# Kernel optimization log

Hardware: AMD Instinct MI355X
Metric: run time of the kernel (lower is better)

The kernel has to match this reference:

```python
import jax, jax.numpy as jnp
import numpy as np

N = 4096          # total ensemble boxes per frame
M = 20            # MAX_MERGE_NUMS
H = 16            # MergeNet hidden_c
COND_THRES = 0.2
IOU_THRES = 0.3


def setup_inputs() -> dict:
    key = jax.random.key(0)
    ks = jax.random.split(key, 6)
    u = jax.random.uniform(ks[0], (N, 9), dtype=jnp.float32)
    # realistic lidar boxes: centers in a ~140x80x8m range, dims in [0.5, 4.5), heading in [-pi, pi)
    centers = (u[:, 0:3] - 0.5) * jnp.array([140.0, 80.0, 8.0], jnp.float32)
    dims = u[:, 3:6] * 4.0 + 0.5
    heading = (u[:, 6:7] - 0.5) * (2.0 * np.pi)
    extra = u[:, 7:9]  # extra box attrs (cols 7:9), untouched by merge
    pred_boxes = jnp.concatenate([centers, dims, heading, extra], axis=-1)
    pred_scores = jax.random.uniform(ks[1], (N,), dtype=jnp.float32)
    pred_labels = jax.random.randint(ks[2], (N,), 0, 3)
    w1 = (jax.random.normal(ks[3], (M, H), jnp.float32) / np.sqrt(M)).astype(jnp.float32)
    b1 = jnp.zeros((H,), jnp.float32)
    w2 = (jax.random.normal(ks[4], (H, H), jnp.float32) / np.sqrt(H)).astype(jnp.float32)
    b2 = jnp.zeros((H,), jnp.float32)
    w3 = (jax.random.normal(ks[5], (H, 1), jnp.float32) / np.sqrt(H)).astype(jnp.float32)
    b3 = jnp.zeros((1,), jnp.float32)
    return dict(pred_boxes=pred_boxes, pred_scores=pred_scores, pred_labels=pred_labels,
                w1=w1, b1=b1, w2=w2, b2=b2, w3=w3, b3=b3)


def _bev_aligned(b):
    # boxes3d_lidar_to_aligned_bev_boxes: swap dx/dy when |limit_period(heading)| >= pi/4
    ang = b[..., 6] - jnp.floor(b[..., 6] / np.pi + 0.5) * np.pi
    swap = jnp.abs(ang) >= (np.pi / 4)
    dx = jnp.where(swap, b[..., 4], b[..., 3])
    dy = jnp.where(swap, b[..., 3], b[..., 4])
    return jnp.stack([b[..., 0] - dx / 2, b[..., 1] - dy / 2,
                      b[..., 0] + dx / 2, b[..., 1] + dy / 2], axis=-1)


def _iou_one_many(a, b):
    # axis-aligned BEV IoU of one box a[4] vs many b[N,4]
    xmin = jnp.maximum(a[0], b[:, 0]); ymin = jnp.maximum(a[1], b[:, 1])
    xmax = jnp.minimum(a[2], b[:, 2]); ymax = jnp.minimum(a[3], b[:, 3])
    inter = jnp.maximum(xmax - xmin, 0.0) * jnp.maximum(ymax - ymin, 0.0)
    area_a = (a[2] - a[0]) * (a[3] - a[1])
    area_b = (b[:, 2] - b[:, 0]) * (b[:, 3] - b[:, 1])
    return inter / jnp.maximum(area_a + area_b - inter, 1e-6)


def _nms_merge(pred_boxes, pred_scores, pred_labels, w1, b1, w2, b2, w3, b3):
    valid = pred_scores > COND_THRES
    sort_key = jnp.where(valid, pred_scores, -jnp.inf)
    order = jnp.argsort(-sort_key)                 # descending by score; invalid sink
    boxes9 = pred_boxes[order]
    labels = pred_labels[order]
    scores = pred_scores[order]
    suppressed0 = ~valid[order]
    boxes7 = boxes9[:, :7]
    bev0 = _bev_aligned(boxes7)                    # merged boxes get suppressed, so bev is static

    def mergenet(ob):                              # ob: [M, 7] -> merged box [7]
        x = ob.T                                   # [7, M] (k is the feature axis)
        h = jax.nn.relu(x @ w1 + b1)
        h = jax.nn.relu(h @ w2 + b2)
        return (h @ w3 + b3)[:, 0]

    def step(suppressed, i):
        active = ~suppressed[i]
        same = (labels == labels[i]) & (~suppressed)
        iou = _iou_one_many(bev0[i], bev0)         # [N]
        over = (iou > IOU_THRES) & same            # includes self (iou=1)
        count = jnp.sum(over)
        rank = jnp.cumsum(over) - 1                # slot of each overlap, in score order
        tgt = jnp.where(over & (rank < M), rank, M)
        ob = jnp.zeros((M, 7), boxes7.dtype).at[tgt].set(boxes7, mode='drop')
        bi = boxes7[i]
        new_box = jnp.where(count > 1, mergenet(ob), bi)
        new_box = new_box.at[3:6].set(jnp.maximum(new_box[3:6], 1e-5))
        out_box = jnp.where(active, new_box, bi)
        return suppressed | (over & active), (out_box, active)

    _, (merged7, keep) = jax.lax.scan(step, suppressed0, jnp.arange(N))
    out_boxes = jnp.concatenate([merged7, boxes9[:, 7:9]], axis=-1)   # [N, 9]
    return out_boxes, scores, labels, keep


def reference(pred_boxes, pred_scores, pred_labels, w1, b1, w2, b2, w3, b3):
    # Returns fixed-shape (boxes9, scores, labels, keep_mask); rows with keep=False
    # correspond to boxes that torch's dynamic version would have removed.
    return _nms_merge(pred_boxes, pred_scores, pred_labels, w1, b1, w2, b2, w3, b3)
```

## Files before the change

### kernel.cpp

```cpp
#include <hip/hip_runtime.h>
#include <cstdint>

typedef unsigned long long u64;
typedef unsigned int u32;

#define NB 4096
#define NW 64
#define MM 20
#define HH 16
#define COND_THRES 0.2f
#define IOU_THRES 0.3f
#define PI_F  3.14159265358979323846f
#define PI4_F 0.78539816339744830962f

#define WS_KEPT    0
#define WS_MASK    32768
#define WS_BOX9S   (WS_MASK + NB*NW*8)
#define WS_BEVS    (WS_BOX9S + NB*9*4)
#define WS_SCORES  (WS_BEVS + NB*16)
#define WS_LABELS  (WS_SCORES + NB*4)
#define WS_NBRW    (WS_LABELS + NB*4)
#define WS_SUPSTEP (WS_NBRW + NB*8)

__device__ __forceinline__ u64 sort_key(float s, int i) {
  u32 sb = (s > COND_THRES) ? __float_as_uint(s) : 0u;
  return ((u64)(sb ^ 0xFFFFFFFFu) << 12) | (u64)i;
}

__global__ void __launch_bounds__(256) k_prep(const float* __restrict__ scores,
                                              const float* __restrict__ boxes9,
                                              const int* __restrict__ labels,
                                              float* __restrict__ box9s, float4* __restrict__ bevs,
                                              float* __restrict__ scoress, int* __restrict__ labelss,
                                              u64* __restrict__ nbrw) {
  #pragma clang fp contract(off)
  __shared__ u64 keys[NB];
  __shared__ u32 part[16][16];
  int tid = threadIdx.x;
  for (int k = tid; k < NB; k += 256) keys[k] = sort_key(scores[k], k);
  __syncthreads();
  int bl = tid & 15;
  int ch = tid >> 4;
  u64 ki = keys[blockIdx.x * 16 + bl];
  int c = 0;
  #pragma unroll 16
  for (int t = 0; t < 256; ++t) c += (keys[(ch << 8) + t] < ki) ? 1 : 0;
  part[bl][ch] = (u32)c;
  __syncthreads();
  if (tid < 16) {
    int i = blockIdx.x * 16 + tid;
    int r = 0;
    #pragma unroll
    for (int q = 0; q < 16; ++q) r += (int)part[tid][q];
    nbrw[i] = 0;
    float b[9];
    #pragma unroll
    for (int f = 0; f < 9; ++f) b[f] = boxes9[i * 9 + f];
    #pragma unroll
    for (int f = 0; f < 9; ++f) box9s[r * 9 + f] = b[f];
    float ang = b[6] - floorf(b[6] / PI_F + 0.5f) * PI_F;
    bool sw = fabsf(ang) >= PI4_F;
    float dx = sw ? b[4] : b[3];
    float dy = sw ? b[3] : b[4];
    bevs[r] = make_float4(b[0] - dx * 0.5f, b[1] - dy * 0.5f,
                          b[0] + dx * 0.5f, b[1] + dy * 0.5f);
    scoress[r] = scores[i];
    labelss[r] = labels[i];
  }
}

__global__ void __launch_bounds__(64) k_mask(const float4* __restrict__ bevs,
                                             const int* __restrict__ labelss,
                                             const float* __restrict__ scoress,
                                             u64* __restrict__ mask,
                                             u64* __restrict__ nbrw) {
  #pragma clang fp contract(off)
  __shared__ float4 bj[64];
  __shared__ int lj[64];
  __shared__ u64 tw[64];
  int t = threadIdx.x;
  int b = blockIdx.x;
  int it = (int)((sqrtf(8.0f * (float)b + 1.0f) - 1.0f) * 0.5f);
  while ((it + 1) * (it + 2) / 2 <= b) ++it;
  while (it * (it + 1) / 2 > b) --it;
  int jt = b - it * (it + 1) / 2;
  int j = jt * 64 + t;
  bj[t] = bevs[j];
  lj[t] = labelss[j];
  u64 vj = __ballot(scoress[j] > COND_THRES);
  int i = it * 64 + t;
  float4 a = bevs[i];
  int la = labelss[i];
  float area_a = (a.z - a.x) * (a.w - a.y);
  __syncthreads();
  u64 w = 0;
  #pragma unroll 8
  for (int kk = 0; kk < 64; ++kk) {
    float4 bb = bj[kk];
    float xmin = fmaxf(a.x, bb.x), ymin = fmaxf(a.y, bb.y);
    float xmax = fminf(a.z, bb.z), ymax = fminf(a.w, bb.w);
    float inter = fmaxf(xmax - xmin, 0.0f) * fmaxf(ymax - ymin, 0.0f);
    float area_b = (bb.z - bb.x) * (bb.w - bb.y);
    float iou = inter / fmaxf(area_a + area_b - inter, 1e-6f);
    if ((iou > IOU_THRES) && (la == lj[kk])) w |= (1ull << kk);
  }
  mask[(u64)i * NW + jt] = w;
  {
    u64 below = (jt < it) ? ~0ull : ((1ull << t) - 1ull);
    if (w & vj & below) atomicOr(&nbrw[i], 1ull << jt);
  }
  if (jt < it) {
    tw[t] = w;
    __syncthreads();
    u64 wT = 0;
    #pragma unroll 8
    for (int k = 0; k < 64; ++k) wT |= ((tw[k] >> t) & 1ull) << k;
    mask[(u64)j * NW + it] = wT;
  }
}

__global__ void __launch_bounds__(1024) k_nms(const u64* __restrict__ mask,
                                              const u64* __restrict__ nbrw,
                                              const float* __restrict__ scoress,
                                              int* __restrict__ supstep) {
  __shared__ u64 decided[64], kept[64];
  __shared__ int wavePending[16];
  int tid = threadIdx.x;
  int lane = tid & 63;
  int waveId = tid >> 6;
  bool validB[4];
  #pragma unroll
  for (int s = 0; s < 4; ++s) {
    int i = tid + (s << 10);
    bool v = scoress[i] > COND_THRES;
    validB[s] = v;
    u64 vw = __ballot(v);
    if (lane == 0) {
      decided[waveId + (s << 4)] = ~vw;
      kept[waveId + (s << 4)] = 0;
    }
  }
  u64 cw0[4], cw1[4];
  u32 meta[4];
  #pragma unroll
  for (int s = 0; s < 4; ++s) {
    int i = tid + (s << 10);
    int wi = i >> 6;
    u64 bit = 1ull << (i & 63);
    u64 t = nbrw[i];
    int n = 0; u32 ovf = 0;
    u64 c0 = 0, c1 = 0; u32 i0 = 0, i1 = 0;
    while (t) {
      int w = __builtin_ctzll(t);
      t &= t - 1;
      u64 below = (w < wi) ? ~0ull : (bit - 1ull);
      u64 m = mask[(u64)i * NW + w] & below;
      if (n == 0)      { c0 = m; i0 = (u32)w; }
      else if (n == 1) { c1 = m; i1 = (u32)w; }
      else ovf = 1;
      ++n;
    }
    cw0[s] = c0; cw1[s] = c1;
    meta[s] = i0 | (i1 << 6) | ((u32)(n > 2 ? 2 : n) << 12) | (ovf << 14);
  }
  __syncthreads();
  for (int s = 0; s < 4; ++s) {
    const int i = tid + (s << 10);
    const int wi = waveId + (s << 4);
    const u64 bit = 1ull << (i & 63);
    const u32 mt = meta[s];
    bool und = validB[s];
    while (true) {
      bool dec = false, keepme = false;
      if (und) {
        bool hasU = false, hasK = false;
        if (!(mt & (1u << 14))) {
          int n = (mt >> 12) & 3;
          if (n >= 1) {
            int w = mt & 63;
            u64 dw = decided[w], kw = kept[w];
            hasU = (cw0[s] & ~dw) != 0ull;
            hasK = (cw0[s] & kw) != 0ull;
          }
          if (n >= 2) {
            int w = (mt >> 6) & 63;
            u64 dw = decided[w], kw = kept[w];
            hasU = hasU || ((cw1[s] & ~dw) != 0ull);
            hasK = hasK || ((cw1[s] & kw) != 0ull);
          }
        } else {
          u64 t = nbrw[i];
          while (t) {
            int w = __builtin_ctzll(t);
            t &= t - 1;
            u64 below = (w < wi) ? ~0ull : (bit - 1ull);
            u64 m = mask[(u64)i * NW + w] & below;
            hasU = hasU || ((m & ~decided[w]) != 0ull);
            hasK = hasK || ((m & kept[w]) != 0ull);
          }
        }
        dec = !hasU;
        keepme = !hasK;
      }
      u64 b_nd = __ballot(dec);
      u64 b_nk = __ballot(dec && keepme);
      bool pend = und && !dec;
      u64 pw = __ballot(pend);
      if (lane == 0) {
        decided[wi] |= b_nd;
        kept[wi] |= b_nk;
        wavePending[waveId] = (pw != 0ull) ? 1 : 0;
      }
      und = pend;
      __syncthreads();
      int any = 0;
      #pragma unroll
      for (int w = 0; w < 16; ++w) any |= wavePending[w];
      if (!any) break;
    }
  }
  #pragma unroll
  for (int s = 0; s < 4; ++s) {
    int j = tid + (s << 10);
    int res;
    if (!validB[s]) {
      res = -1;
    } else {
      res = j;
      u32 mt = meta[s];
      if (!(mt & (1u << 14))) {
        int n = (mt >> 12) & 3;
        if (n >= 1) {
          int w0 = mt & 63;
          u64 m0 = cw0[s] & kept[w0];
          if (m0) {
            res = (w0 << 6) + __builtin_ctzll(m0);
          } else if (n >= 2) {
            int w1 = (mt >> 6) & 63;
            u64 m1 = cw1[s] & kept[w1];
            if (m1) res = (w1 << 6) + __builtin_ctzll(m1);
          }
        }
      } else {
        int wj = j >> 6;
        u64 bitbelow = (1ull << (j & 63)) - 1ull;
        u64 t = nbrw[j];
        while (t) {
          int w = __builtin_ctzll(t);
          t &= t - 1;
          u64 m = mask[(u64)j * NW + w] & kept[w];
          if (w == wj) m &= bitbelow;
          if (m) { res = (w << 6) + __builtin_ctzll(m); break; }
        }
      }
    }
    supstep[j] = res;
  }
}

__global__ void __launch_bounds__(64) k_merge(
    const u64* __restrict__ mask, const int* __restrict__ supstep,
    const float* __restrict__ box9s, const float* __restrict__ scoress,
    const int* __restrict__ labelss,
    const float* __restrict__ w1, const float* __restrict__ b1,
    const float* __restrict__ w2, const float* __restrict__ b2,
    const float* __restrict__ w3, const float* __restrict__ b3,
    float* __restrict__ out) {
  #pragma clang fp contract(off)
  __shared__ int candList[MM];
  __shared__ float ob[MM][7];
  __shared__ float h1[7][HH];
  __shared__ float h2[7][HH];
  __shared__ float res[7];
  int i = blockIdx.x;
  int t = threadIdx.x;
  bool active = (supstep[i] == i);
  u64 wq = 0;
  int cnt = 0;
  if (active) {
    u64 w = mask[(u64)i * NW + t];
    while (w) {
      int b = __builtin_ctzll(w);
      w &= w - 1;
      int j = (t << 6) | b;
      if (supstep[j] >= i) { wq |= (1ull << b); cnt++; }
    }
  }
  int incl = cnt;
  #pragma unroll
  for (int off = 1; off < 64; off <<= 1) {
    int v = __shfl_up(incl, off);
    if (t >= off) incl += v;
  }
  int excl = incl - cnt;
  int count = __shfl(incl, 63);
  bool merged = active && (count > 1);
  if (merged && wq) {
    int pos = excl;
    u64 ww = wq;
    while (ww && pos < MM) {
      int b = __builtin_ctzll(ww);
      ww &= ww - 1;
      candList[pos++] = (t << 6) | b;
    }
  }
  __syncthreads();
  if (merged) {
    int nc = count < MM ? count : MM;
    if (t < MM) {
      if (t < nc) {
        int j = candList[t];
        #pragma unroll
        for (int f = 0; f < 7; ++f) ob[t][f] = box9s[j * 9 + f];
      } else {
        #pragma unroll
        for (int f = 0; f < 7; ++f) ob[t][f] = 0.0f;
      }
    }
    __syncthreads();
    for (int o = t; o < 7 * HH; o += 64) {
      int f = o >> 4, hh = o & 15;
      float acc = b1[hh];
      #pragma unroll
      for (int m = 0; m < MM; ++m) acc += ob[m][f] * w1[m * HH + hh];
      h1[f][hh] = fmaxf(acc, 0.0f);
    }
    __syncthreads();
    for (int o = t; o < 7 * HH; o += 64) {
      int f = o >> 4, oo = o & 15;
      float acc = b2[oo];
      #pragma unroll
      for (int k = 0; k < HH; ++k) acc += h1[f][k] * w2[k * HH + oo];
      h2[f][oo] = fmaxf(acc, 0.0f);
    }
    __syncthreads();
    if (t < 7) {
      float acc = b3[0];
      #pragma unroll
      for (int k = 0; k < HH; ++k) acc += h2[t][k] * w3[k];
      if (t >= 3 && t < 6) acc = fmaxf(acc, 1e-5f);
      res[t] = acc;
    }
    __syncthreads();
  }
  if (t < 9) {
    float v = box9s[i * 9 + t];
    if (merged && t < 7) v = res[t];
    out[i * 9 + t] = v;
  }
  if (t == 0) {
    out[NB * 9 + i]          = scoress[i];
    out[NB * 9 + NB + i]     = (float)labelss[i];
    out[NB * 9 + 2 * NB + i] = active ? 1.0f : 0.0f;
  }
}

extern "C" void kernel_launch(void* const* d_in, const int* in_sizes, int n_in,
                              void* d_out, int out_size, void* d_ws, size_t ws_size,
                              hipStream_t stream) {
  const float* boxes9 = (const float*)d_in[0];
  const float* scores = (const float*)d_in[1];
  const int*   labels = (const int*)d_in[2];
  const float* w1 = (const float*)d_in[3];
  const float* b1 = (const float*)d_in[4];
  const float* w2 = (const float*)d_in[5];
  const float* b2 = (const float*)d_in[6];
  const float* w3 = (const float*)d_in[7];
  const float* b3 = (const float*)d_in[8];
  char* ws = (char*)d_ws;
  u64*    mask    = (u64*)(ws + WS_MASK);
  float*  box9s   = (float*)(ws + WS_BOX9S);
  float4* bevs    = (float4*)(ws + WS_BEVS);
  float*  scoress = (float*)(ws + WS_SCORES);
  int*    labelss = (int*)(ws + WS_LABELS);
  u64*    nbrw    = (u64*)(ws + WS_NBRW);
  int*    supstep = (int*)(ws + WS_SUPSTEP);
  float*  out     = (float*)d_out;

  hipLaunchKernelGGL(k_prep,  dim3(256),  dim3(256),  0, stream,
                     scores, boxes9, labels, box9s, bevs, scoress, labelss, nbrw);
  hipLaunchKernelGGL(k_mask,  dim3(2080), dim3(64),   0, stream,
                     bevs, labelss, scoress, mask, nbrw);
  hipLaunchKernelGGL(k_nms,   dim3(1),    dim3(1024), 0, stream,
                     mask, nbrw, scoress, supstep);
  hipLaunchKernelGGL(k_merge, dim3(NB),   dim3(64),   0, stream,
                     mask, supstep, box9s, scoress, labelss,
                     w1, b1, w2, b2, w3, b3, out);
}
```

Baseline: 111.9 us.

## Fuse mask and NMS kernels using a last-block-done atomic counter

Merges the IoU mask kernel and the single-block NMS kernel into one launch. Each 1024-thread block computes 16 triangular tiles (one per wave), then increments a global done counter, and the last block to finish runs the greedy NMS pass. This removes one kernel launch and its inter-kernel gap. In exchange, the 130 blocks hold 1024 threads each, and correctness depends on the release/acquire fences and on the counter being reset in k_prep.

```diff
diff --git a/kernel.cpp b/kernel.cpp
--- a/kernel.cpp
+++ b/kernel.cpp
@@ -13,7 +13,10 @@
 #define PI_F  3.14159265358979323846f
 #define PI4_F 0.78539816339744830962f
 
-#define WS_KEPT    0
+#define NTILE 2080
+#define MASK_BLOCKS 130
+
+#define WS_DONE    0
 #define WS_MASK    32768
 #define WS_BOX9S   (WS_MASK + NB*NW*8)
 #define WS_BEVS    (WS_BOX9S + NB*9*4)
@@ -32,12 +35,13 @@
                                               const int* __restrict__ labels,
                                               float* __restrict__ box9s, float4* __restrict__ bevs,
                                               float* __restrict__ scoress, int* __restrict__ labelss,
-                                              u64* __restrict__ nbrw) {
+                                              u64* __restrict__ nbrw, u32* __restrict__ doneCnt) {
   #pragma clang fp contract(off)
   __shared__ u64 keys[NB];
   __shared__ u32 part[16][16];
   int tid = threadIdx.x;
   for (int k = tid; k < NB; k += 256) keys[k] = sort_key(scores[k], k);
+  if (blockIdx.x == 0 && tid == 0) atomicExch(doneCnt, 0u);
   __syncthreads();
   int bl = tid & 15;
   int ch = tid >> 4;
@@ -69,65 +73,75 @@
   }
 }
 
-__global__ void __launch_bounds__(64) k_mask(const float4* __restrict__ bevs,
-                                             const int* __restrict__ labelss,
-                                             const float* __restrict__ scoress,
-                                             u64* __restrict__ mask,
-                                             u64* __restrict__ nbrw) {
+__global__ void __launch_bounds__(1024) k_masknms(
+    const float4* __restrict__ bevs, const int* __restrict__ labelss,
+    const float* __restrict__ scoress,
+    u64* __restrict__ mask, u64* __restrict__ nbrw,
+    const u64* __restrict__ nbrw_c, int* __restrict__ supstep,
+    u32* __restrict__ doneCnt) {
   #pragma clang fp contract(off)
-  __shared__ float4 bj[64];
-  __shared__ int lj[64];
-  __shared__ u64 tw[64];
-  int t = threadIdx.x;
-  int b = blockIdx.x;
-  int it = (int)((sqrtf(8.0f * (float)b + 1.0f) - 1.0f) * 0.5f);
-  while ((it + 1) * (it + 2) / 2 <= b) ++it;
-  while (it * (it + 1) / 2 > b) --it;
-  int jt = b - it * (it + 1) / 2;
-  int j = jt * 64 + t;
-  bj[t] = bevs[j];
-  lj[t] = labelss[j];
-  u64 vj = __ballot(scoress[j] > COND_THRES);
-  int i = it * 64 + t;
-  float4 a = bevs[i];
-  int la = labelss[i];
-  float area_a = (a.z - a.x) * (a.w - a.y);
-  __syncthreads();
-  u64 w = 0;
-  #pragma unroll 8
-  for (int kk = 0; kk < 64; ++kk) {
-    float4 bb = bj[kk];
-    float xmin = fmaxf(a.x, bb.x), ymin = fmaxf(a.y, bb.y);
-    float xmax = fminf(a.z, bb.z), ymax = fminf(a.w, bb.w);
-    float inter = fmaxf(xmax - xmin, 0.0f) * fmaxf(ymax - ymin, 0.0f);
-    float area_b = (bb.z - bb.x) * (bb.w - bb.y);
-    float iou = inter / fmaxf(area_a + area_b - inter, 1e-6f);
-    if ((iou > IOU_THRES) && (la == lj[kk])) w |= (1ull << kk);
-  }
-  mask[(u64)i * NW + jt] = w;
-  {
-    u64 below = (jt < it) ? ~0ull : ((1ull << t) - 1ull);
-    if (w & vj & below) atomicOr(&nbrw[i], 1ull << jt);
-  }
-  if (jt < it) {
-    tw[t] = w;
-    __syncthreads();
-    u64 wT = 0;
-    #pragma unroll 8
-    for (int k = 0; k < 64; ++k) wT |= ((tw[k] >> t) & 1ull) << k;
-    mask[(u64)j * NW + it] = wT;
-  }
-}
-
-__global__ void __launch_bounds__(1024) k_nms(const u64* __restrict__ mask,
-                                              const u64* __restrict__ nbrw,
-                                              const float* __restrict__ scoress,
-                                              int* __restrict__ supstep) {
+  __shared__ float4 bj[16][64];
+  __shared__ int    lj[16][64];
+  __shared__ u64    tw[16][64];
   __shared__ u64 decided[64], kept[64];
   __shared__ int wavePending[16];
-  int tid = threadIdx.x;
-  int lane = tid & 63;
-  int waveId = tid >> 6;
+  __shared__ int isLast;
+  const int tid = threadIdx.x;
+  const int lane = tid & 63;
+  const int waveId = tid >> 6;
+
+  {
+    int T = (blockIdx.x << 4) | waveId;
+    int it = (int)((sqrtf(8.0f * (float)T + 1.0f) - 1.0f) * 0.5f);
+    while ((it + 1) * (it + 2) / 2 <= T) ++it;
+    while (it * (it + 1) / 2 > T) --it;
+    int jt = T - it * (it + 1) / 2;
+    int j = jt * 64 + lane;
+    bj[waveId][lane] = bevs[j];
+    lj[waveId][lane] = labelss[j];
+    u64 vj = __ballot(scoress[j] > COND_THRES);
+    int i = it * 64 + lane;
+    float4 a = bevs[i];
+    int la = labelss[i];
+    float area_a = (a.z - a.x) * (a.w - a.y);
+    __syncthreads();
+    u64 w = 0;
+    #pragma unroll 8
+    for (int kk = 0; kk < 64; ++kk) {
+      float4 bb = bj[waveId][kk];
+      float xmin = fmaxf(a.x, bb.x), ymin = fmaxf(a.y, bb.y);
+      float xmax = fminf(a.z, bb.z), ymax = fminf(a.w, bb.w);
+      float inter = fmaxf(xmax - xmin, 0.0f) * fmaxf(ymax - ymin, 0.0f);
+      float area_b = (bb.z - bb.x) * (bb.w - bb.y);
+      float iou = inter / fmaxf(area_a + area_b - inter, 1e-6f);
+      if ((iou > IOU_THRES) && (la == lj[waveId][kk])) w |= (1ull << kk);
+    }
+    mask[(u64)i * NW + jt] = w;
+    {
+      u64 below = (jt < it) ? ~0ull : ((1ull << lane) - 1ull);
+      if (w & vj & below) atomicOr(&nbrw[i], 1ull << jt);
+    }
+    tw[waveId][lane] = w;
+    __syncthreads();
+    if (jt < it) {
+      u64 wT = 0;
+      #pragma unroll 8
+      for (int k = 0; k < 64; ++k) wT |= ((tw[waveId][k] >> lane) & 1ull) << k;
+      mask[(u64)j * NW + it] = wT;
+    }
+  }
+
+  __syncthreads();
+  if (tid == 0) {
+    __builtin_amdgcn_fence(__ATOMIC_RELEASE, "agent");
+    u32 v = atomicAdd(doneCnt, 1u);
+    int last = (v == (u32)(MASK_BLOCKS - 1));
+    if (last) __builtin_amdgcn_fence(__ATOMIC_ACQUIRE, "agent");
+    isLast = last;
+  }
+  __syncthreads();
+  if (!isLast) return;
+
   bool validB[4];
   #pragma unroll
   for (int s = 0; s < 4; ++s) {
@@ -147,7 +161,7 @@
     int i = tid + (s << 10);
     int wi = i >> 6;
     u64 bit = 1ull << (i & 63);
-    u64 t = nbrw[i];
+    u64 t = nbrw_c[i];
     int n = 0; u32 ovf = 0;
     u64 c0 = 0, c1 = 0; u32 i0 = 0, i1 = 0;
     while (t) {
@@ -189,7 +203,7 @@
             hasK = hasK || ((cw1[s] & kw) != 0ull);
           }
         } else {
-          u64 t = nbrw[i];
+          u64 t = nbrw_c[i];
           while (t) {
             int w = __builtin_ctzll(t);
             t &= t - 1;
@@ -244,7 +258,7 @@
       } else {
         int wj = j >> 6;
         u64 bitbelow = (1ull << (j & 63)) - 1ull;
-        u64 t = nbrw[j];
+        u64 t = nbrw_c[j];
         while (t) {
           int w = __builtin_ctzll(t);
           t &= t - 1;
@@ -368,6 +382,7 @@
   const float* w3 = (const float*)d_in[7];
   const float* b3 = (const float*)d_in[8];
   char* ws = (char*)d_ws;
+  u32*    doneCnt = (u32*)(ws + WS_DONE);
   u64*    mask    = (u64*)(ws + WS_MASK);
   float*  box9s   = (float*)(ws + WS_BOX9S);
   float4* bevs    = (float4*)(ws + WS_BEVS);
@@ -377,13 +392,11 @@
   int*    supstep = (int*)(ws + WS_SUPSTEP);
   float*  out     = (float*)d_out;
 
-  hipLaunchKernelGGL(k_prep,  dim3(256),  dim3(256),  0, stream,
-                     scores, boxes9, labels, box9s, bevs, scoress, labelss, nbrw);
-  hipLaunchKernelGGL(k_mask,  dim3(2080), dim3(64),   0, stream,
-                     bevs, labelss, scoress, mask, nbrw);
-  hipLaunchKernelGGL(k_nms,   dim3(1),    dim3(1024), 0, stream,
-                     mask, nbrw, scoress, supstep);
-  hipLaunchKernelGGL(k_merge, dim3(NB),   dim3(64),   0, stream,
+  hipLaunchKernelGGL(k_prep,    dim3(256),         dim3(256),  0, stream,
+                     scores, boxes9, labels, box9s, bevs, scoress, labelss, nbrw, doneCnt);
+  hipLaunchKernelGGL(k_masknms, dim3(MASK_BLOCKS), dim3(1024), 0, stream,
+                     bevs, labelss, scoress, mask, nbrw, nbrw, supstep, doneCnt);
+  hipLaunchKernelGGL(k_merge,   dim3(NB),          dim3(64),   0, stream,
                      mask, supstep, box9s, scoress, labelss,
                      w1, b1, w2, b2, w3, b3, out);
 }
```

Result: slower. 116.2 us (+3.9%).
